# Optimization experiments

Measured on AMD Instinct MI355X. Metric: run time of the kernel, lower is better.

## Reference

```python
import jax, jax.numpy as jnp
import numpy as np

B, N, S = 8, 4096, 1024
D1, D2 = 128, 256
IN_CH, OUT_CH = D1 + D2, 256
BN_EPS = 1e-5


def setup_inputs() -> dict:
    key = jax.random.key(0)
    ks = jax.random.split(key, 12)
    inp = {
        "xyz1": jax.random.normal(ks[0], (B, N, 3), jnp.float32),
        "xyz2": jax.random.normal(ks[1], (B, S, 3), jnp.float32),
        "points1": jax.random.normal(ks[2], (B, N, D1), jnp.float32),
        "points2": jax.random.normal(ks[3], (B, S, D2), jnp.float32),
        # fuse: Conv1d(in_ch->out_ch, k=1) + BN
        "W_fuse": jax.random.normal(ks[4], (OUT_CH, IN_CH), jnp.float32) * (1.0 / np.sqrt(IN_CH)),
        "b_fuse": jnp.zeros((OUT_CH,), jnp.float32),
        "g_fuse": jnp.ones((OUT_CH,), jnp.float32),
        "bt_fuse": jnp.zeros((OUT_CH,), jnp.float32),
        # res block net1: Conv1d(out_ch->out_ch) + BN (res_expansion=1.0)
        "W1": jax.random.normal(ks[5], (OUT_CH, OUT_CH), jnp.float32) * (1.0 / np.sqrt(OUT_CH)),
        "b1": jnp.zeros((OUT_CH,), jnp.float32),
        "g1": jnp.ones((OUT_CH,), jnp.float32),
        "bt1": jnp.zeros((OUT_CH,), jnp.float32),
        # res block net2: Conv1d(out_ch->out_ch) + BN
        "W2": jax.random.normal(ks[6], (OUT_CH, OUT_CH), jnp.float32) * (1.0 / np.sqrt(OUT_CH)),
        "b2": jnp.zeros((OUT_CH,), jnp.float32),
        "g2": jnp.ones((OUT_CH,), jnp.float32),
        "bt2": jnp.zeros((OUT_CH,), jnp.float32),
    }
    return inp


def _bn(x, g, b):
    # BatchNorm1d training-mode forward: stats over (batch, length), x: [B, C, L]
    m = jnp.mean(x, axis=(0, 2), keepdims=True)
    v = jnp.var(x, axis=(0, 2), keepdims=True)
    return (x - m) * jax.lax.rsqrt(v + BN_EPS) * g[None, :, None] + b[None, :, None]


def _conv1x1(x, W, b):
    # x: [B, C_in, L], W: [C_out, C_in] -> [B, C_out, L]
    return jnp.einsum("oc,bcl->bol", W, x) + b[None, :, None]


def _gelu(x):
    return jax.nn.gelu(x, approximate=False)  # torch nn.GELU default (erf)


def reference(xyz1, xyz2, points1, points2,
              W_fuse, b_fuse, g_fuse, bt_fuse,
              W1, b1, g1, bt1, W2, b2, g2, bt2):
    # squared pairwise distances [B, N, S] without B x N x S x 3 intermediate
    d = (jnp.sum(xyz1 * xyz1, -1)[:, :, None]
         - 2.0 * jnp.einsum("bnc,bsc->bns", xyz1, xyz2)
         + jnp.sum(xyz2 * xyz2, -1)[:, None, :])
    # 3 nearest coarse points per dense point (== sort ascending, take first 3)
    neg_d3, idx = jax.lax.top_k(-d, 3)            # [B, N, 3]
    d3 = -neg_d3
    recip = 1.0 / (d3 + 1e-8)
    w = recip / jnp.sum(recip, axis=2, keepdims=True)  # [B, N, 3]
    gathered = points2[jnp.arange(points2.shape[0])[:, None, None], idx]  # [B, N, 3, D2]
    interp = jnp.sum(gathered * w[..., None], axis=2)  # [B, N, D2]

    new_points = jnp.concatenate([points1, interp], axis=-1)  # [B, N, D1+D2]
    x = jnp.transpose(new_points, (0, 2, 1))                   # [B, C, N]

    # fuse: conv-bn-gelu
    x = _gelu(_bn(_conv1x1(x, W_fuse, b_fuse), g_fuse, bt_fuse))
    # residual block: gelu(bn(conv(gelu(bn(conv(x))))) + x)
    y = _gelu(_bn(_conv1x1(x, W1, b1), g1, bt1))
    y = _bn(_conv1x1(y, W2, b2), g2, bt2)
    x = _gelu(y + x)

    return jnp.transpose(x, (0, 2, 1))  # [B, N, out_ch]
```

## Files before the change

kernel.cpp:

```cpp
#include <hip/hip_runtime.h>
#include <hip/hip_bf16.h>

constexpr int Bb = 8, Nn = 4096, Ss = 1024;
constexpr int D1 = 128, D2 = 256, KIN = 384, OC = 256;
constexpr int L = Bb * Nn;
constexpr float BN_EPS = 1e-5f;

typedef __attribute__((ext_vector_type(4))) float floatx4;
typedef __attribute__((ext_vector_type(8))) __bf16 bf16x8;

#define DEV __device__ __forceinline__

DEV float bf2f(unsigned short u) {
    union { unsigned int i; float f; } v; v.i = ((unsigned int)u) << 16; return v.f;
}
DEV unsigned short f2bf(float f) {
    union { float f; unsigned int i; } v; v.f = f;
    unsigned int x = v.i;
    return (unsigned short)((x + 0x7FFFu + ((x >> 16) & 1u)) >> 16);
}
DEV float gelu_f(float x) {
    float u = x * (0.7978845608f + 0.0356774081f * x * x);
    float t = __expf(-2.0f * u);
    return x * __builtin_amdgcn_rcpf(1.0f + t);
}

__global__ void k_probe(const unsigned int* __restrict__ w, int* __restrict__ flag) {
    if (threadIdx.x == 0 && blockIdx.x == 0) {
        int sane = 0;
        for (int i = 0; i < 64; ++i) {
            unsigned int lo = w[i] & 0xFFFFu;
            int e = (int)((lo >> 7) & 0xFF);
            if (e >= 100 && e <= 144) ++sane;
        }
        *flag = (sane >= 48) ? 0 : 1;
    }
}

__global__ void k_zero(float* p) {
    int i = blockIdx.x * 256 + threadIdx.x;
    if (i < 6 * 256) p[i] = 0.0f;
}

__global__ void k_prep_w(const void* __restrict__ src, unsigned short* __restrict__ dst,
                         int n, const int* __restrict__ dflag) {
    int i = blockIdx.x * 256 + threadIdx.x;
    if (i >= n) return;
    if (*dflag) dst[i] = f2bf(((const float*)src)[i]);
    else        dst[i] = ((const unsigned short*)src)[i];
}

__global__ __launch_bounds__(256) void k_nn(const void* __restrict__ xyz1_,
                                            const void* __restrict__ xyz2_,
                                            const int* __restrict__ dflag,
                                            int* __restrict__ nn_idx, float* __restrict__ nn_w) {
    __shared__ alignas(16) float s4[Ss * 4];
    int b = blockIdx.x >> 4;
    int chunk = blockIdx.x & 15;
    int tid = threadIdx.x;
    bool isf = (*dflag != 0);

    if (isf) {
        const float* p2 = (const float*)xyz2_ + (size_t)b * Ss * 3;
        for (int i = tid; i < Ss * 3; i += 256) {
            int s = i / 3, k = i - s * 3;
            s4[s * 4 + k] = p2[i];
        }
    } else {
        const unsigned short* p2 = (const unsigned short*)xyz2_ + (size_t)b * Ss * 3;
        for (int i = tid; i < Ss * 3; i += 256) {
            int s = i / 3, k = i - s * 3;
            s4[s * 4 + k] = bf2f(p2[i]);
        }
    }
    __syncthreads();
    for (int s = tid; s < Ss; s += 256) {
        float x = s4[s * 4], y = s4[s * 4 + 1], z = s4[s * 4 + 2];
        s4[s * 4 + 3] = x * x + y * y + z * z;
    }
    __syncthreads();

    int n = chunk * 256 + tid;
    int bn = b * Nn + n;
    float x1, y1, z1;
    if (isf) {
        const float* p1 = (const float*)xyz1_ + (size_t)bn * 3;
        x1 = p1[0]; y1 = p1[1]; z1 = p1[2];
    } else {
        const unsigned short* p1 = (const unsigned short*)xyz1_ + (size_t)bn * 3;
        x1 = bf2f(p1[0]); y1 = bf2f(p1[1]); z1 = bf2f(p1[2]);
    }
    float n1 = x1 * x1 + y1 * y1 + z1 * z1;

    float d0 = 3.4e38f, d1 = 3.4e38f, d2 = 3.4e38f;
    int i0 = 0, i1 = 0, i2 = 0;
#pragma unroll 4
    for (int s = 0; s < Ss; ++s) {
        float4 q = *(const float4*)&s4[s * 4];
        float d = n1 + q.w - 2.0f * (x1 * q.x + y1 * q.y + z1 * q.z);
        bool c2 = d < d2, c1 = d < d1, c0 = d < d0;
        d2 = c1 ? d1 : (c2 ? d : d2); i2 = c1 ? i1 : (c2 ? s : i2);
        d1 = c0 ? d0 : (c1 ? d : d1); i1 = c0 ? i0 : (c1 ? s : i1);
        d0 = c0 ? d  : d0;            i0 = c0 ? s  : i0;
    }
    float r0 = 1.0f / (d0 + 1e-8f), r1 = 1.0f / (d1 + 1e-8f), r2 = 1.0f / (d2 + 1e-8f);
    float rs = 1.0f / (r0 + r1 + r2);
    nn_idx[bn * 3 + 0] = i0; nn_idx[bn * 3 + 1] = i1; nn_idx[bn * 3 + 2] = i2;
    nn_w[bn * 3 + 0] = r0 * rs; nn_w[bn * 3 + 1] = r1 * rs; nn_w[bn * 3 + 2] = r2 * rs;
}

__global__ __launch_bounds__(256) void k_build_x(const void* __restrict__ points1_,
                                                 const void* __restrict__ points2_,
                                                 const int* __restrict__ dflag,
                                                 const int* __restrict__ nn_idx,
                                                 const float* __restrict__ nn_w,
                                                 unsigned short* __restrict__ X) {
    int tid = threadIdx.x;
    int pt = blockIdx.x * 4 + (tid >> 6);
    int lane = tid & 63;
    int b = pt >> 12;
    bool isf = (*dflag != 0);

    int i0 = nn_idx[pt * 3], i1 = nn_idx[pt * 3 + 1], i2 = nn_idx[pt * 3 + 2];
    float w0 = nn_w[pt * 3], w1 = nn_w[pt * 3 + 1], w2 = nn_w[pt * 3 + 2];
    int c = lane * 4;

    if (isf) {
        const float* p1 = (const float*)points1_ + (size_t)pt * D1;
        float2 v = *(const float2*)(p1 + lane * 2);
        unsigned int packed = (unsigned int)f2bf(v.x) | ((unsigned int)f2bf(v.y) << 16);
        ((unsigned int*)(X + (size_t)pt * KIN))[lane] = packed;

        const float* base = (const float*)points2_;
        const float* r0 = base + ((size_t)(b * Ss + i0)) * D2 + c;
        const float* r1 = base + ((size_t)(b * Ss + i1)) * D2 + c;
        const float* r2 = base + ((size_t)(b * Ss + i2)) * D2 + c;
        float4 a0 = *(const float4*)r0;
        float4 a1 = *(const float4*)r1;
        float4 a2 = *(const float4*)r2;
        uint2 out;
        unsigned short* uo = (unsigned short*)&out;
        uo[0] = f2bf(w0 * a0.x + w1 * a1.x + w2 * a2.x);
        uo[1] = f2bf(w0 * a0.y + w1 * a1.y + w2 * a2.y);
        uo[2] = f2bf(w0 * a0.z + w1 * a1.z + w2 * a2.z);
        uo[3] = f2bf(w0 * a0.w + w1 * a1.w + w2 * a2.w);
        *(uint2*)(X + (size_t)pt * KIN + D1 + c) = out;
    } else {
        const unsigned short* p1 = (const unsigned short*)points1_;
        ((unsigned int*)(X + (size_t)pt * KIN))[lane] =
            ((const unsigned int*)(p1 + (size_t)pt * D1))[lane];

        const unsigned short* base = (const unsigned short*)points2_;
        const unsigned short* r0 = base + ((size_t)(b * Ss + i0)) * D2 + c;
        const unsigned short* r1 = base + ((size_t)(b * Ss + i1)) * D2 + c;
        const unsigned short* r2 = base + ((size_t)(b * Ss + i2)) * D2 + c;
        uint2 v0 = *(const uint2*)r0;
        uint2 v1 = *(const uint2*)r1;
        uint2 v2 = *(const uint2*)r2;
        const unsigned short* u0 = (const unsigned short*)&v0;
        const unsigned short* u1 = (const unsigned short*)&v1;
        const unsigned short* u2 = (const unsigned short*)&v2;
        uint2 out;
        unsigned short* uo = (unsigned short*)&out;
#pragma unroll
        for (int j = 0; j < 4; ++j)
            uo[j] = f2bf(w0 * bf2f(u0[j]) + w1 * bf2f(u1[j]) + w2 * bf2f(u2[j]));
        *(uint2*)(X + (size_t)pt * KIN + D1 + c) = out;
    }
}

template <int K, int ACT>
__global__ __launch_bounds__(256) void k_gemm(const unsigned short* __restrict__ A,
                                              const unsigned short* __restrict__ W,
                                              unsigned short* __restrict__ Out,
                                              float* __restrict__ S1, float* __restrict__ S2,
                                              const float* __restrict__ cA,
                                              const float* __restrict__ cC) {
    __shared__ alignas(16) unsigned short As[128 * 64];
    __shared__ alignas(16) unsigned short Bs[128 * 64];
    __shared__ float sS1[128], sS2[128];

    int tid = threadIdx.x;
    int l0 = blockIdx.x * 128;
    int o0 = blockIdx.y * 128;
    int wave = tid >> 6, lane = tid & 63, quad = lane >> 4, lr = lane & 15;
    int wm = wave >> 1, wn = wave & 1;

    floatx4 zero4 = {0.f, 0.f, 0.f, 0.f};
    floatx4 acc[4][4];
#pragma unroll
    for (int mi = 0; mi < 4; ++mi)
#pragma unroll
        for (int ni = 0; ni < 4; ++ni) acc[mi][ni] = zero4;

    constexpr int KC = K / 64;
    for (int kc = 0; kc < KC; ++kc) {
        __syncthreads();
#pragma unroll
        for (int it = 0; it < 4; ++it) {
            int idx = it * 256 + tid;
            int row = idx >> 3, c8 = idx & 7;
            union { uint4 v; unsigned short u[8]; } va;
            va.v = *(const uint4*)(A + (size_t)(l0 + row) * K + kc * 64 + c8 * 8);
            if (ACT) {
                int kbase = kc * 64 + c8 * 8;
#pragma unroll
                for (int j = 0; j < 8; ++j) {
                    float f = bf2f(va.u[j]);
                    va.u[j] = f2bf(gelu_f(cA[kbase + j] * f + cC[kbase + j]));
                }
            }
            *(uint4*)&As[row * 64 + ((c8 ^ (row & 7)) << 3)] = va.v;

            uint4 vb = *(const uint4*)(W + (size_t)(o0 + row) * K + kc * 64 + c8 * 8);
            *(uint4*)&Bs[row * 64 + ((c8 ^ (row & 7)) << 3)] = vb;
        }
        __syncthreads();
#pragma unroll
        for (int ks8 = 0; ks8 < 2; ++ks8) {
            bf16x8 af[4], bfr[4];
#pragma unroll
            for (int mi = 0; mi < 4; ++mi) {
                int ra = wm * 64 + mi * 16 + lr;
                af[mi] = *(const bf16x8*)&As[ra * 64 + ((((ks8 << 2) + quad) ^ (ra & 7)) << 3)];
            }
#pragma unroll
            for (int ni = 0; ni < 4; ++ni) {
                int rb = wn * 64 + ni * 16 + lr;
                bfr[ni] = *(const bf16x8*)&Bs[rb * 64 + ((((ks8 << 2) + quad) ^ (rb & 7)) << 3)];
            }
#pragma unroll
            for (int mi = 0; mi < 4; ++mi)
#pragma unroll
                for (int ni = 0; ni < 4; ++ni)
                    acc[mi][ni] = __builtin_amdgcn_mfma_f32_16x16x32_bf16(af[mi], bfr[ni], acc[mi][ni], 0, 0, 0);
        }
    }

    float p1[4] = {0, 0, 0, 0}, p2[4] = {0, 0, 0, 0};
#pragma unroll
    for (int mi = 0; mi < 4; ++mi) {
#pragma unroll
        for (int ni = 0; ni < 4; ++ni) {
#pragma unroll
            for (int r = 0; r < 4; ++r) {
                float v = acc[mi][ni][r];
                int row = l0 + wm * 64 + mi * 16 + quad * 4 + r;
                int col = o0 + wn * 64 + ni * 16 + lr;
                Out[(size_t)row * OC + col] = f2bf(v);
                p1[ni] += v;
                p2[ni] += v * v;
            }
        }
    }
    if (tid < 128) { sS1[tid] = 0.f; sS2[tid] = 0.f; }
    __syncthreads();
#pragma unroll
    for (int ni = 0; ni < 4; ++ni) {
        atomicAdd(&sS1[wn * 64 + ni * 16 + lr], p1[ni]);
        atomicAdd(&sS2[wn * 64 + ni * 16 + lr], p2[ni]);
    }
    __syncthreads();
    if (tid < 128) {
        atomicAdd(&S1[o0 + tid], sS1[tid]);
        atomicAdd(&S2[o0 + tid], sS2[tid]);
    }
}

__global__ void k_finalize(const float* __restrict__ S1, const float* __restrict__ S2,
                           const void* __restrict__ g_, const void* __restrict__ bt_,
                           const int* __restrict__ dflag,
                           float* __restrict__ cA, float* __restrict__ cC) {
    int o = threadIdx.x;
    float m = S1[o] * (1.0f / (float)L);
    float var = S2[o] * (1.0f / (float)L) - m * m;
    float g, bt;
    if (*dflag) { g = ((const float*)g_)[o]; bt = ((const float*)bt_)[o]; }
    else { g = bf2f(((const unsigned short*)g_)[o]); bt = bf2f(((const unsigned short*)bt_)[o]); }
    float a = g * rsqrtf(var + BN_EPS);
    cA[o] = a;
    cC[o] = bt - m * a;
}

__global__ __launch_bounds__(256) void k_final(const unsigned short* __restrict__ t0,
                                               const unsigned short* __restrict__ t2,
                                               const float* __restrict__ cA0, const float* __restrict__ cC0,
                                               const float* __restrict__ cA2, const float* __restrict__ cC2,
                                               const int* __restrict__ dflag,
                                               void* __restrict__ out_) {
    int idx = (blockIdx.x * 256 + threadIdx.x) * 8;
    int col = idx & (OC - 1);
    union { uint4 v; unsigned short u[8]; } v0, v2;
    v0.v = *(const uint4*)(t0 + idx);
    v2.v = *(const uint4*)(t2 + idx);
    float r[8];
#pragma unroll
    for (int j = 0; j < 8; ++j) {
        float x = gelu_f(cA0[col + j] * bf2f(v0.u[j]) + cC0[col + j]);
        float y = cA2[col + j] * bf2f(v2.u[j]) + cC2[col + j];
        r[j] = gelu_f(x + y);
    }
    if (*dflag) {
        float* o = (float*)out_ + idx;
        float4 lo = {r[0], r[1], r[2], r[3]};
        float4 hi = {r[4], r[5], r[6], r[7]};
        *(float4*)o = lo;
        *(float4*)(o + 4) = hi;
    } else {
        union { uint4 v; unsigned short u[8]; } vo;
#pragma unroll
        for (int j = 0; j < 8; ++j) vo.u[j] = f2bf(r[j]);
        *(uint4*)((unsigned short*)out_ + idx) = vo.v;
    }
}

extern "C" void kernel_launch(void* const* d_in, const int* in_sizes, int n_in,
                              void* d_out, int out_size, void* d_ws, size_t ws_size,
                              hipStream_t stream) {
    const void* xyz1    = d_in[0];
    const void* xyz2    = d_in[1];
    const void* points1 = d_in[2];
    const void* points2 = d_in[3];
    const void* W_fuse  = d_in[4];
    const void* g_fuse  = d_in[6];
    const void* bt_fuse = d_in[7];
    const void* W1      = d_in[8];
    const void* g1      = d_in[10];
    const void* bt1     = d_in[11];
    const void* W2      = d_in[12];
    const void* g2      = d_in[14];
    const void* bt2     = d_in[15];

    char* ws = (char*)d_ws;
    unsigned short* X  = (unsigned short*)ws;
    unsigned short* t0 = (unsigned short*)(ws + 25165824);
    unsigned short* t1 = (unsigned short*)d_out;
    unsigned short* t2 = X;
    int*   nn_idx = (int*)(ws + 41943040);
    float* nn_w   = (float*)(ws + 42336256);
    float* stats  = (float*)(ws + 42729472);
    int*   dflag  = (int*)(ws + 42729472 + 3072 * 4);
    unsigned short* Wf_bf = (unsigned short*)(ws + 42745856);
    unsigned short* W1_bf = Wf_bf + 256 * KIN;
    unsigned short* W2_bf = W1_bf + 256 * OC;

    float *S1_0 = stats,        *S2_0 = stats + 256;
    float *S1_1 = stats + 512,  *S2_1 = stats + 768;
    float *S1_2 = stats + 1024, *S2_2 = stats + 1280;
    float *cA0 = stats + 1536, *cC0 = stats + 1792;
    float *cA1 = stats + 2048, *cC1 = stats + 2304;
    float *cA2 = stats + 2560, *cC2 = stats + 2816;

    k_probe<<<1, 64, 0, stream>>>((const unsigned int*)xyz1, dflag);
    k_zero<<<6, 256, 0, stream>>>(stats);
    k_prep_w<<<(256 * KIN + 255) / 256, 256, 0, stream>>>(W_fuse, Wf_bf, 256 * KIN, dflag);
    k_prep_w<<<(256 * OC + 255) / 256, 256, 0, stream>>>(W1, W1_bf, 256 * OC, dflag);
    k_prep_w<<<(256 * OC + 255) / 256, 256, 0, stream>>>(W2, W2_bf, 256 * OC, dflag);
    k_nn<<<128, 256, 0, stream>>>(xyz1, xyz2, dflag, nn_idx, nn_w);
    k_build_x<<<L / 4, 256, 0, stream>>>(points1, points2, dflag, nn_idx, nn_w, X);

    dim3 ggrid(L / 128, 2);
    k_gemm<KIN, 0><<<ggrid, 256, 0, stream>>>(X, Wf_bf, t0, S1_0, S2_0, nullptr, nullptr);
    k_finalize<<<1, 256, 0, stream>>>(S1_0, S2_0, g_fuse, bt_fuse, dflag, cA0, cC0);
    k_gemm<OC, 1><<<ggrid, 256, 0, stream>>>(t0, W1_bf, t1, S1_1, S2_1, cA0, cC0);
    k_finalize<<<1, 256, 0, stream>>>(S1_1, S2_1, g1, bt1, dflag, cA1, cC1);
    k_gemm<OC, 1><<<ggrid, 256, 0, stream>>>(t1, W2_bf, t2, S1_2, S2_2, cA1, cC1);
    k_finalize<<<1, 256, 0, stream>>>(S1_2, S2_2, g2, bt2, dflag, cA2, cC2);
    k_final<<<L * OC / (256 * 8), 256, 0, stream>>>(t0, t2, cA0, cC0, cA2, cC2, dflag, d_out);
}
```

Before: 279.1 us.

## Split KNN search across 8 lanes per point and merge top-3 via shuffles

The nearest-neighbour kernel now assigns 8 threads per dense point, each scanning 128 coarse points, then merges the partial top-3 lists with xor-shuffles, using a tie-break that keeps the lower index. The grid grows from 128 blocks to 1024, which fills more compute units, whereas before there was only one block per 256 points. Shared memory gets padding every 128 entries so the 8 lanes of a point read different banks. The cost is that every block reloads xyz2 into LDS (8x more total loads) and the shuffle-merge adds work.

```diff
diff --git a/kernel.cpp b/kernel.cpp
--- a/kernel.cpp
+++ b/kernel.cpp
@@ -50,38 +50,56 @@
     else        dst[i] = ((const unsigned short*)src)[i];
 }
 
+DEV void merge3(float& d0, float& d1, float& d2, int& i0, int& i1, int& i2,
+                float e0, float e1, float e2, int j0, int j1, int j2, bool pref) {
+    float a0 = d0, a1 = d1, a2 = d2; int x0 = i0, x1 = i1, x2 = i2;
+    float b0 = e0, b1 = e1;          int y0 = j0, y1 = j1;
+    bool t = pref ? (a0 <= b0) : (a0 < b0);
+    d0 = t ? a0 : b0; i0 = t ? x0 : y0;
+    a0 = t ? a1 : a0; x0 = t ? x1 : x0;
+    a1 = t ? a2 : a1; x1 = t ? x2 : x1;
+    b0 = t ? b0 : b1; y0 = t ? y0 : y1;
+    b1 = t ? b1 : e2; y1 = t ? y1 : j2;
+    t = pref ? (a0 <= b0) : (a0 < b0);
+    d1 = t ? a0 : b0; i1 = t ? x0 : y0;
+    a0 = t ? a1 : a0; x0 = t ? x1 : x0;
+    b0 = t ? b0 : b1; y0 = t ? y0 : y1;
+    t = pref ? (a0 <= b0) : (a0 < b0);
+    d2 = t ? a0 : b0; i2 = t ? x0 : y0;
+}
+
 __global__ __launch_bounds__(256) void k_nn(const void* __restrict__ xyz1_,
                                             const void* __restrict__ xyz2_,
                                             const int* __restrict__ dflag,
                                             int* __restrict__ nn_idx, float* __restrict__ nn_w) {
-    __shared__ alignas(16) float s4[Ss * 4];
-    int b = blockIdx.x >> 4;
-    int chunk = blockIdx.x & 15;
+    __shared__ alignas(16) float s4[Ss * 4 + 32];
     int tid = threadIdx.x;
+    int b = (blockIdx.x * 32) >> 12;
     bool isf = (*dflag != 0);
 
     if (isf) {
         const float* p2 = (const float*)xyz2_ + (size_t)b * Ss * 3;
         for (int i = tid; i < Ss * 3; i += 256) {
             int s = i / 3, k = i - s * 3;
-            s4[s * 4 + k] = p2[i];
+            s4[s * 4 + k + ((s >> 7) << 2)] = p2[i];
         }
     } else {
         const unsigned short* p2 = (const unsigned short*)xyz2_ + (size_t)b * Ss * 3;
         for (int i = tid; i < Ss * 3; i += 256) {
             int s = i / 3, k = i - s * 3;
-            s4[s * 4 + k] = bf2f(p2[i]);
+            s4[s * 4 + k + ((s >> 7) << 2)] = bf2f(p2[i]);
         }
     }
     __syncthreads();
     for (int s = tid; s < Ss; s += 256) {
-        float x = s4[s * 4], y = s4[s * 4 + 1], z = s4[s * 4 + 2];
-        s4[s * 4 + 3] = x * x + y * y + z * z;
+        int a = s * 4 + ((s >> 7) << 2);
+        float x = s4[a], y = s4[a + 1], z = s4[a + 2];
+        s4[a + 3] = x * x + y * y + z * z;
     }
     __syncthreads();
 
-    int n = chunk * 256 + tid;
-    int bn = b * Nn + n;
+    int part = tid & 7;
+    int bn = blockIdx.x * 32 + (tid >> 3);
     float x1, y1, z1;
     if (isf) {
         const float* p1 = (const float*)xyz1_ + (size_t)bn * 3;
@@ -94,19 +112,30 @@
 
     float d0 = 3.4e38f, d1 = 3.4e38f, d2 = 3.4e38f;
     int i0 = 0, i1 = 0, i2 = 0;
+    const float* sp = &s4[part * 516];
 #pragma unroll 4
-    for (int s = 0; s < Ss; ++s) {
-        float4 q = *(const float4*)&s4[s * 4];
+    for (int j = 0; j < 128; ++j) {
+        float4 q = *(const float4*)(sp + j * 4);
         float d = n1 + q.w - 2.0f * (x1 * q.x + y1 * q.y + z1 * q.z);
+        int s = part * 128 + j;
         bool c2 = d < d2, c1 = d < d1, c0 = d < d0;
         d2 = c1 ? d1 : (c2 ? d : d2); i2 = c1 ? i1 : (c2 ? s : i2);
         d1 = c0 ? d0 : (c1 ? d : d1); i1 = c0 ? i0 : (c1 ? s : i1);
         d0 = c0 ? d  : d0;            i0 = c0 ? s  : i0;
     }
-    float r0 = 1.0f / (d0 + 1e-8f), r1 = 1.0f / (d1 + 1e-8f), r2 = 1.0f / (d2 + 1e-8f);
-    float rs = 1.0f / (r0 + r1 + r2);
-    nn_idx[bn * 3 + 0] = i0; nn_idx[bn * 3 + 1] = i1; nn_idx[bn * 3 + 2] = i2;
-    nn_w[bn * 3 + 0] = r0 * rs; nn_w[bn * 3 + 1] = r1 * rs; nn_w[bn * 3 + 2] = r2 * rs;
+#pragma unroll
+    for (int m = 1; m <= 4; m <<= 1) {
+        float e0 = __shfl_xor(d0, m, 64), e1 = __shfl_xor(d1, m, 64), e2 = __shfl_xor(d2, m, 64);
+        int   j0 = __shfl_xor(i0, m, 64), j1 = __shfl_xor(i1, m, 64), j2 = __shfl_xor(i2, m, 64);
+        bool pref = (part < (part ^ m));
+        merge3(d0, d1, d2, i0, i1, i2, e0, e1, e2, j0, j1, j2, pref);
+    }
+    if (part == 0) {
+        float r0 = 1.0f / (d0 + 1e-8f), r1 = 1.0f / (d1 + 1e-8f), r2 = 1.0f / (d2 + 1e-8f);
+        float rs = 1.0f / (r0 + r1 + r2);
+        nn_idx[bn * 3 + 0] = i0; nn_idx[bn * 3 + 1] = i1; nn_idx[bn * 3 + 2] = i2;
+        nn_w[bn * 3 + 0] = r0 * rs; nn_w[bn * 3 + 1] = r1 * rs; nn_w[bn * 3 + 2] = r2 * rs;
+    }
 }
 
 __global__ __launch_bounds__(256) void k_build_x(const void* __restrict__ points1_,
@@ -356,7 +385,7 @@
     k_prep_w<<<(256 * KIN + 255) / 256, 256, 0, stream>>>(W_fuse, Wf_bf, 256 * KIN, dflag);
     k_prep_w<<<(256 * OC + 255) / 256, 256, 0, stream>>>(W1, W1_bf, 256 * OC, dflag);
     k_prep_w<<<(256 * OC + 255) / 256, 256, 0, stream>>>(W2, W2_bf, 256 * OC, dflag);
-    k_nn<<<128, 256, 0, stream>>>(xyz1, xyz2, dflag, nn_idx, nn_w);
+    k_nn<<<L / 32, 256, 0, stream>>>(xyz1, xyz2, dflag, nn_idx, nn_w);
     k_build_x<<<L / 4, 256, 0, stream>>>(points1, points2, dflag, nn_idx, nn_w, X);
 
     dim3 ggrid(L / 128, 2);
```

Result: faster. 245.8 us (-11.9%).
